# Kernel tuning notes

Measured on AMD Instinct MI355X. Metric: run time of the kernel, lower is better.

Reference implementation:

```python
import math
import jax, jax.numpy as jnp
import numpy as np

HIDDEN = 1024
HEADS = 16
HEAD = HIDDEN // HEADS
BUCKET = 32
MAXPOS = 512
REL = 2 * BUCKET - 1
EPS = 1e-7
L, B = 512, 16
STD = math.sqrt(2.0 / (5.0 * HIDDEN))


def _ln(x, g=None, b=None):
    m = x.mean(-1, keepdims=True)
    v = ((x - m) ** 2).mean(-1, keepdims=True)
    y = (x - m) * jax.lax.rsqrt(v + EPS)
    return y if g is None else y * g + b


def _bucket_indices(n):
    # DeBERTa-style log bucket relative positions, shifted to [0, 2*BUCKET-2]
    r = jnp.arange(n)[:, None] - jnp.arange(n)[None, :]
    mid = BUCKET // 2
    abs_pos = jnp.where((r < mid) & (r > -mid), mid - 1,
                        jnp.clip(jnp.abs(r), None, MAXPOS - 1))
    log_pos = jnp.ceil(jnp.log(abs_pos.astype(jnp.float32) / mid)
                       / math.log((MAXPOS - 1) / mid) * (mid - 1)).astype(jnp.int32) + mid
    bucket_pos = jnp.where(abs_pos <= mid, r, log_pos * jnp.sign(r))
    return (BUCKET - 1 + bucket_pos).astype(jnp.int32)


def setup_inputs() -> dict:
    key = jax.random.key(0)
    ks = jax.random.split(key, 8)
    return {
        'hidden_states': jax.random.normal(ks[0], (L, B, HIDDEN), jnp.float32),
        'attention_mask': jax.random.randint(ks[1], (B, 1, 1, L), 0, 2).astype(bool),
        'relative_embedding': jax.random.normal(ks[2], (REL, HIDDEN), jnp.float32),
        'wqk': jax.random.normal(ks[3], (2 * HIDDEN, HIDDEN), jnp.float32) * STD,
        'bqk': jnp.zeros((2 * HIDDEN,), jnp.float32),
        'wv': jax.random.normal(ks[4], (HIDDEN, HIDDEN), jnp.float32) * STD,
        'bv': jnp.zeros((HIDDEN,), jnp.float32),
        'wo': jax.random.normal(ks[5], (HIDDEN, HIDDEN), jnp.float32) * STD,
        'bo': jnp.zeros((HIDDEN,), jnp.float32),
        'ln_g': jnp.ones((HIDDEN,), jnp.float32),
        'ln_b': jnp.zeros((HIDDEN,), jnp.float32),
    }


def reference(hidden_states, attention_mask, relative_embedding,
              wqk, bqk, wv, bv, wo, bo, ln_g, ln_b):
    Lq, Bq, D = hidden_states.shape
    scale = 1.0 / math.sqrt(3 * HEAD)
    h = _ln(hidden_states)                                 # pre LN, no affine
    q, k = jnp.split(h @ wqk.T + bqk, 2, axis=-1)
    v = h @ wv.T + bv
    qpos, kpos = jnp.split(relative_embedding @ wqk.T + bqk, 2, axis=-1)
    qpos = qpos.reshape(REL, HEADS, HEAD)
    kpos = kpos.reshape(REL, HEADS, HEAD)
    # (L,B,D) -> (B,H,L,hd)
    qh = q.reshape(Lq, Bq, HEADS, HEAD).transpose(1, 2, 0, 3)
    kh = k.reshape(Lq, Bq, HEADS, HEAD).transpose(1, 2, 0, 3)
    vh = v.reshape(Lq, Bq, HEADS, HEAD).transpose(1, 2, 0, 3)
    scores = jnp.einsum('bhqd,bhkd->bhqk', qh, kh) * scale       # c2c
    qp = jnp.einsum('bhqd,khd->bhqk', qh, kpos) * scale          # c2p (k over buckets)
    pk = jnp.einsum('bhkd,qhd->bhqk', kh, qpos) * scale          # p2c (q over buckets)
    idx = jnp.broadcast_to(_bucket_indices(Lq), (Bq, HEADS, Lq, Lq))
    scores = scores + jnp.take_along_axis(qp, idx, axis=-1) \
                    + jnp.take_along_axis(pk, idx, axis=-2)
    # masked softmax: mask==True -> -inf before softmax, 0 after
    probs = jax.nn.softmax(jnp.where(attention_mask, -1e9, scores), axis=-1)
    probs = jnp.where(attention_mask, 0.0, probs)
    ctx = jnp.einsum('bhqk,bhkd->bhqd', probs, vh)
    ctx = ctx.transpose(2, 0, 1, 3).reshape(Lq, Bq, D)           # (L,B,D)
    out = ctx @ wo.T + bo
    return _ln(out, ln_g, ln_b)
```

## Files before the change

### kernel.cpp

```cpp
#include <hip/hip_runtime.h>
#include <hip/hip_bf16.h>

#define HID 1024
#define HEADS 16
#define HEAD 64
#define RELN 63
#define SEQ 512
#define BATCH 16
#define NROWS (SEQ*BATCH)
#define MEXT 8320
#define NQKV 3072
#define LNEPS 1e-7f

typedef __attribute__((ext_vector_type(4))) float  f32x4;
typedef __attribute__((ext_vector_type(8))) short  s16x8;
typedef __attribute__((ext_vector_type(4))) ushort u16x4;

static __device__ __forceinline__ ushort f2bf(float f) {
  union { float f; unsigned u; } v; v.f = f;
  unsigned r = v.u + 0x7fffu + ((v.u >> 16) & 1u);
  return (ushort)(r >> 16);
}
static __device__ __forceinline__ float bf2f(ushort u) {
  union { unsigned u; float f; } v; v.u = ((unsigned)u) << 16;
  return v.f;
}

__global__ void k_prep(const void* mask_raw, const float* bqk, const float* bv,
                       ushort* mask01, int* idx_tab, float* bcat) {
  __shared__ int s_isbool;
  int tid = threadIdx.x;
  if (tid == 0) s_isbool = 0;
  __syncthreads();
  const unsigned* mu = (const unsigned*)mask_raw;
  int bad = 0;
  for (int i = tid; i < 2048; i += 256) if (mu[i] > 1u) bad = 1;
  if (bad) s_isbool = 1;
  __syncthreads();
  int isbool = s_isbool;
  const unsigned char* m8 = (const unsigned char*)mask_raw;
  const int* m32 = (const int*)mask_raw;
  for (int i = tid; i < BATCH*SEQ; i += 256) {
    int m = isbool ? (int)m8[i] : m32[i];
    mask01[i] = m ? 1 : 0;
  }
  for (int i = tid; i < 1023; i += 256) {
    int r = i - 511;
    int a = r < 0 ? -r : r;
    int absp = (a < 16) ? 15 : (a < 511 ? a : 511);
    int idx;
    if (absp <= 16) idx = 31 + r;
    else {
      float v = logf((float)absp / 16.0f) / logf(511.0f / 16.0f) * 15.0f;
      int lp = (int)ceilf(v) + 16;
      idx = 31 + (r > 0 ? lp : -lp);
    }
    idx_tab[i] = idx;
  }
  for (int i = tid; i < 2048; i += 256) bcat[i] = bqk[i];
  for (int i = tid; i < 1024; i += 256) bcat[2048 + i] = bv[i];
}

__global__ void k_convert(const float* wqk, const float* wv, const float* wo,
                          ushort* wcat, ushort* wo_b) {
  int i = blockIdx.x * 256 + threadIdx.x;
  if (i < 2048 * 1024) wcat[i] = f2bf(wqk[i]);
  else if (i < 3072 * 1024) wcat[i] = f2bf(wv[i - 2048 * 1024]);
  if (i < 1024 * 1024) wo_b[i] = f2bf(wo[i]);
}

__global__ __launch_bounds__(256) void k_ln1(const float* hid, const float* rel, ushort* h_ext) {
  int row = blockIdx.x, tid = threadIdx.x;
  __shared__ float red[8];
  if (row < NROWS) {
    const float* src = hid + (size_t)row * HID;
    f32x4 x = *(const f32x4*)(src + tid * 4);
    float s = x[0] + x[1] + x[2] + x[3];
    #pragma unroll
    for (int m = 1; m < 64; m <<= 1) s += __shfl_xor(s, m);
    if ((tid & 63) == 0) red[tid >> 6] = s;
    __syncthreads();
    float mean = (red[0] + red[1] + red[2] + red[3]) * (1.0f / HID);
    float d0 = x[0] - mean, d1 = x[1] - mean, d2 = x[2] - mean, d3 = x[3] - mean;
    float sq = d0*d0 + d1*d1 + d2*d2 + d3*d3;
    #pragma unroll
    for (int m = 1; m < 64; m <<= 1) sq += __shfl_xor(sq, m);
    __syncthreads();
    if ((tid & 63) == 0) red[4 + (tid >> 6)] = sq;
    __syncthreads();
    float var = (red[4] + red[5] + red[6] + red[7]) * (1.0f / HID);
    float rs = rsqrtf(var + LNEPS);
    u16x4 o = { f2bf(d0*rs), f2bf(d1*rs), f2bf(d2*rs), f2bf(d3*rs) };
    *(u16x4*)(h_ext + (size_t)row * HID + tid * 4) = o;
  } else if (row < NROWS + RELN) {
    const float* src = rel + (size_t)(row - NROWS) * HID;
    f32x4 x = *(const f32x4*)(src + tid * 4);
    u16x4 o = { f2bf(x[0]), f2bf(x[1]), f2bf(x[2]), f2bf(x[3]) };
    *(u16x4*)(h_ext + (size_t)row * HID + tid * 4) = o;
  } else {
    u16x4 z = { 0, 0, 0, 0 };
    *(u16x4*)(h_ext + (size_t)row * HID + tid * 4) = z;
  }
}

template<int WRITE_F32>
__global__ __launch_bounds__(256) void k_gemm(const ushort* A, const ushort* Bw, const float* bias,
                                              ushort* Cb, float* Cf, int M, int N, int K) {
  __shared__ char smem[32768];
  char* As = smem;
  char* Bs = smem + 16384;
  int tid = threadIdx.x, lane = tid & 63, w = tid >> 6;
  int nbn = N >> 7;
  int per = gridDim.x >> 3;
  int gl = (blockIdx.x & 7) * per + (blockIdx.x >> 3);
  int bm = gl / nbn, bn = gl % nbn;
  int wr = w >> 1, wc = w & 1;
  int g = lane >> 4, r = lane & 15;
  f32x4 acc[4][4] = {};
  for (int ko = 0; ko < K; ko += 64) {
    __syncthreads();
    #pragma unroll
    for (int c = 0; c < 4; ++c) {
      int chunk = c * 256 + tid;
      int row = chunk >> 3;
      int kb = (chunk & 7) << 4;
      int kbs = kb ^ ((row & 7) << 4);
      const char* gA = (const char*)(A + (size_t)(bm * 128 + row) * K + ko) + kbs;
      const char* gB = (const char*)(Bw + (size_t)(bn * 128 + row) * K + ko) + kbs;
      __builtin_amdgcn_global_load_lds((const __attribute__((address_space(1))) void*)gA,
                                       (__attribute__((address_space(3))) void*)(As + c * 4096 + w * 1024),
                                       16, 0, 0);
      __builtin_amdgcn_global_load_lds((const __attribute__((address_space(1))) void*)gB,
                                       (__attribute__((address_space(3))) void*)(Bs + c * 4096 + w * 1024),
                                       16, 0, 0);
    }
    __syncthreads();
    #pragma unroll
    for (int kk = 0; kk < 2; ++kk) {
      s16x8 af[4], bf[4];
      #pragma unroll
      for (int mt = 0; mt < 4; ++mt) {
        int row = wr * 64 + mt * 16 + r;
        int kb = (kk * 64 + g * 16) ^ ((row & 7) << 4);
        af[mt] = *(const s16x8*)(As + row * 128 + kb);
      }
      #pragma unroll
      for (int nt = 0; nt < 4; ++nt) {
        int row = wc * 64 + nt * 16 + r;
        int kb = (kk * 64 + g * 16) ^ ((row & 7) << 4);
        bf[nt] = *(const s16x8*)(Bs + row * 128 + kb);
      }
      #pragma unroll
      for (int mt = 0; mt < 4; ++mt)
        #pragma unroll
        for (int nt = 0; nt < 4; ++nt)
          acc[mt][nt] = __builtin_amdgcn_mfma_f32_16x16x32_bf16(af[mt], bf[nt], acc[mt][nt], 0, 0, 0);
    }
  }
  #pragma unroll
  for (int nt = 0; nt < 4; ++nt) {
    int col = bn * 128 + wc * 64 + nt * 16 + r;
    float bvv = bias[col];
    #pragma unroll
    for (int mt = 0; mt < 4; ++mt) {
      int row0 = bm * 128 + wr * 64 + mt * 16 + g * 4;
      #pragma unroll
      for (int i = 0; i < 4; ++i) {
        float v = acc[mt][nt][i] + bvv;
        if (WRITE_F32) Cf[(size_t)(row0 + i) * N + col] = v;
        else           Cb[(size_t)(row0 + i) * N + col] = f2bf(v);
      }
    }
  }
}

__global__ __launch_bounds__(256) void k_pos(const ushort* qkv, ushort* qp, ushort* pk) {
  int bh = blockIdx.x;
  int b = bh >> 4, h = bh & 15;
  int tid = threadIdx.x, lane = tid & 63, w = tid >> 6;
  int g = lane >> 4, r = lane & 15;
  s16x8 bkp[4][2], bqp[4][2];
  #pragma unroll
  for (int nt = 0; nt < 4; ++nt)
    #pragma unroll
    for (int kk = 0; kk < 2; ++kk) {
      size_t rowp = (size_t)(NROWS + nt * 16 + r);
      int colq = h * 64 + kk * 32 + g * 8;
      bqp[nt][kk] = *(const s16x8*)(qkv + rowp * NQKV + colq);
      bkp[nt][kk] = *(const s16x8*)(qkv + rowp * NQKV + 1024 + colq);
    }
  for (int cc = 0; cc < 8; ++cc) {
    int rowbase = cc * 64 + w * 16;
    s16x8 aq[2], ak[2];
    #pragma unroll
    for (int kk = 0; kk < 2; ++kk) {
      size_t rowq = (size_t)((rowbase + r) * 16 + b);
      int colq = h * 64 + kk * 32 + g * 8;
      aq[kk] = *(const s16x8*)(qkv + rowq * NQKV + colq);
      ak[kk] = *(const s16x8*)(qkv + rowq * NQKV + 1024 + colq);
    }
    f32x4 accq[4] = {}, acck[4] = {};
    #pragma unroll
    for (int kk = 0; kk < 2; ++kk)
      #pragma unroll
      for (int nt = 0; nt < 4; ++nt) {
        accq[nt] = __builtin_amdgcn_mfma_f32_16x16x32_bf16(aq[kk], bkp[nt][kk], accq[nt], 0, 0, 0);
        acck[nt] = __builtin_amdgcn_mfma_f32_16x16x32_bf16(ak[kk], bqp[nt][kk], acck[nt], 0, 0, 0);
      }
    #pragma unroll
    for (int nt = 0; nt < 4; ++nt)
      #pragma unroll
      for (int i = 0; i < 4; ++i) {
        int q = rowbase + g * 4 + i;
        int t = nt * 16 + r;
        qp[(size_t)bh * SEQ * 64 + q * 64 + t] = f2bf(accq[nt][i]);
        pk[(size_t)bh * SEQ * 64 + q * 64 + t] = f2bf(acck[nt][i]);
      }
  }
}

__global__ __launch_bounds__(256) void k_vt(const ushort* qkv, ushort* vt, ushort* kc) {
  int bid = blockIdx.x;
  int bh = bid >> 3, lt = bid & 7;
  int b = bh >> 4, h = bh & 15;
  __shared__ ushort tile[64][72];
  int tid = threadIdx.x;
  #pragma unroll
  for (int c = 0; c < 2; ++c) {
    int e = (c * 256 + tid) * 8;
    int l = e >> 6, d0 = e & 63;
    size_t row = (size_t)((lt * 64 + l) * 16 + b);
    s16x8 kv = *(const s16x8*)(qkv + row * NQKV + 1024 + h * 64 + d0);
    *(s16x8*)(kc + ((size_t)bh * SEQ + lt * 64 + l) * 64 + d0) = kv;
    *(s16x8*)&tile[l][d0] = *(const s16x8*)(qkv + row * NQKV + 2048 + h * 64 + d0);
  }
  __syncthreads();
  #pragma unroll
  for (int c = 0; c < 2; ++c) {
    int e = (c * 256 + tid) * 8;
    int d = e >> 6, l0 = e & 63;
    ushort tmp[8];
    #pragma unroll
    for (int j = 0; j < 8; ++j) tmp[j] = tile[l0 + j][d];
    *(s16x8*)(vt + (size_t)(bh * 64 + d) * SEQ + lt * 64 + l0) = *(s16x8*)tmp;
  }
}

__global__ __launch_bounds__(256) void k_attn(const ushort* qkv, const ushort* qp_all, const ushort* pk_all,
                                              const ushort* kc, const ushort* vt, const ushort* mask01,
                                              const int* idx_tab, ushort* ctx) {
  int bid = blockIdx.x;
  int slot = bid >> 3;
  int bh = (bid & 7) * 32 + (slot >> 3);
  int qt = slot & 7;
  int b = bh >> 4, h = bh & 15;
  int tid = threadIdx.x, lane = tid & 63, w = tid >> 6;
  int g = lane >> 4, r = lane & 15;

  __shared__ ushort qp_s[64][66];
  __shared__ ushort pk_s[2][64][66];
  __shared__ char   Ks[2][8192];
  __shared__ ushort p_s[4][16][72];
  __shared__ ushort mb_s[512];
  __shared__ ushort idx_s[1024];
  char* Ksp = (char*)Ks;

  const size_t qp_base = (size_t)bh * SEQ * 64 + (size_t)qt * 4096;
  const size_t pk_base = (size_t)bh * SEQ * 64;
  const char* kcb = (const char*)(kc + (size_t)bh * SEQ * 64);

  int krow = w * 8 + (lane >> 3);
  int ksrccol = (((lane & 7) ^ (lane >> 3)) << 4);

  #pragma unroll
  for (int c = 0; c < 2; ++c) {
    const char* src = kcb + (size_t)(c * 32 + krow) * 128 + ksrccol;
    __builtin_amdgcn_global_load_lds((const __attribute__((address_space(1))) void*)src,
                                     (__attribute__((address_space(3))) void*)(Ksp + c * 4096 + w * 1024),
                                     16, 0, 0);
  }
  s16x8 pkreg[2];
  #pragma unroll
  for (int c = 0; c < 2; ++c)
    pkreg[c] = *(const s16x8*)(pk_all + pk_base + (size_t)(c * 256 + tid) * 8);
  #pragma unroll
  for (int c = 0; c < 2; ++c) {
    int chunk = c * 256 + tid;
    s16x8 v = *(const s16x8*)(qp_all + qp_base + (size_t)chunk * 8);
    *(s16x8*)&qp_s[chunk >> 3][(chunk & 7) * 8] = v;
  }
  for (int i = tid; i < 512; i += 256) mb_s[i] = mask01[b * SEQ + i];
  for (int i = tid; i < 1023; i += 256) idx_s[i] = (ushort)idx_tab[i];
  s16x8 aq[2];
  int qg0 = qt * 64 + w * 16;
  #pragma unroll
  for (int kk = 0; kk < 2; ++kk) {
    size_t row = (size_t)((qg0 + r) * 16 + b);
    aq[kk] = *(const s16x8*)(qkv + row * NQKV + h * 64 + kk * 32 + g * 8);
  }
  #pragma unroll
  for (int c = 0; c < 2; ++c) {
    int chunk = c * 256 + tid;
    *(s16x8*)&pk_s[0][chunk >> 3][(chunk & 7) * 8] = pkreg[c];
  }
  __syncthreads();

  float m_i[4], l_i[4];
  f32x4 o_acc[4] = {};
  #pragma unroll
  for (int i = 0; i < 4; ++i) { m_i[i] = -3e38f; l_i[i] = 0.0f; }
  const float scale = 0.07216878364870323f;

  #pragma unroll 2
  for (int kt = 0; kt < 8; ++kt) {
    const int cur = kt & 1;
    if (kt < 7) {
      #pragma unroll
      for (int c = 0; c < 2; ++c) {
        const char* src = kcb + (size_t)(kt + 1) * 8192 + (size_t)(c * 32 + krow) * 128 + ksrccol;
        __builtin_amdgcn_global_load_lds((const __attribute__((address_space(1))) void*)src,
                                         (__attribute__((address_space(3))) void*)(Ksp + (cur ^ 1) * 8192 + c * 4096 + w * 1024),
                                         16, 0, 0);
      }
      #pragma unroll
      for (int c = 0; c < 2; ++c)
        pkreg[c] = *(const s16x8*)(pk_all + pk_base + (size_t)(kt + 1) * 4096 + (size_t)(c * 256 + tid) * 8);
    }

    const char* Kc = Ksp + cur * 8192;
    f32x4 s[4];
    #pragma unroll
    for (int nt = 0; nt < 4; ++nt) {
      f32x4 a = {};
      #pragma unroll
      for (int kk = 0; kk < 2; ++kk) {
        s16x8 bk = *(const s16x8*)(Kc + (nt * 16 + r) * 128 + ((kk * 64 + g * 16) ^ ((r & 7) << 4)));
        a = __builtin_amdgcn_mfma_f32_16x16x32_bf16(aq[kk], bk, a, 0, 0, 0);
      }
      s[nt] = a;
    }

    s16x8 vreg[2][4];
    #pragma unroll
    for (int kk = 0; kk < 2; ++kk)
      #pragma unroll
      for (int nt = 0; nt < 4; ++nt)
        vreg[kk][nt] = *(const s16x8*)(vt + (size_t)(bh * 64 + nt * 16 + r) * SEQ + kt * 64 + kk * 32 + g * 8);

    float p[4][4], tilemax[4];
    #pragma unroll
    for (int i = 0; i < 4; ++i) tilemax[i] = -3e38f;
    #pragma unroll
    for (int nt = 0; nt < 4; ++nt) {
      int kl = nt * 16 + r;
      int kgl = kt * 64 + kl;
      ushort mb = mb_s[kgl];
      #pragma unroll
      for (int i = 0; i < 4; ++i) {
        int ql = w * 16 + g * 4 + i;
        int ridx = (qt * 64 + ql) - kgl + 511;
        int t = idx_s[ridx];
        float v = (s[nt][i] + bf2f(qp_s[ql][t]) + bf2f(pk_s[cur][kl][t])) * scale;
        v = mb ? -3e38f : v;
        s[nt][i] = v;
        tilemax[i] = fmaxf(tilemax[i], v);
      }
    }
    #pragma unroll
    for (int i = 0; i < 4; ++i) {
      float v = tilemax[i];
      v = fmaxf(v, __shfl_xor(v, 1));
      v = fmaxf(v, __shfl_xor(v, 2));
      v = fmaxf(v, __shfl_xor(v, 4));
      v = fmaxf(v, __shfl_xor(v, 8));
      tilemax[i] = v;
    }
    float rs_i[4], psum[4];
    #pragma unroll
    for (int i = 0; i < 4; ++i) {
      float mnew = fmaxf(m_i[i], tilemax[i]);
      rs_i[i] = __expf(m_i[i] - mnew);
      m_i[i] = mnew;
      l_i[i] *= rs_i[i];
      psum[i] = 0.0f;
    }
    #pragma unroll
    for (int nt = 0; nt < 4; ++nt)
      #pragma unroll
      for (int i = 0; i < 4; ++i) {
        float v = s[nt][i];
        float pe = (v <= -1e37f) ? 0.0f : __expf(v - m_i[i]);
        p[nt][i] = pe;
        psum[i] += pe;
      }
    #pragma unroll
    for (int i = 0; i < 4; ++i) {
      float v = psum[i];
      v += __shfl_xor(v, 1);
      v += __shfl_xor(v, 2);
      v += __shfl_xor(v, 4);
      v += __shfl_xor(v, 8);
      l_i[i] += v;
    }
    #pragma unroll
    for (int nt = 0; nt < 4; ++nt)
      #pragma unroll
      for (int i = 0; i < 4; ++i) o_acc[nt][i] *= rs_i[i];

    #pragma unroll
    for (int nt = 0; nt < 4; ++nt)
      #pragma unroll
      for (int i = 0; i < 4; ++i) p_s[w][g * 4 + i][nt * 16 + r] = f2bf(p[nt][i]);

    #pragma unroll
    for (int kk = 0; kk < 2; ++kk) {
      s16x8 pa = *(const s16x8*)&p_s[w][r][kk * 32 + g * 8];
      #pragma unroll
      for (int nt = 0; nt < 4; ++nt)
        o_acc[nt] = __builtin_amdgcn_mfma_f32_16x16x32_bf16(pa, vreg[kk][nt], o_acc[nt], 0, 0, 0);
    }

    if (kt < 7) {
      #pragma unroll
      for (int c = 0; c < 2; ++c) {
        int chunk = c * 256 + tid;
        *(s16x8*)&pk_s[cur ^ 1][chunk >> 3][(chunk & 7) * 8] = pkreg[c];
      }
    }
    __syncthreads();
  }

  #pragma unroll
  for (int i = 0; i < 4; ++i) {
    float inv = l_i[i] > 0.0f ? 1.0f / l_i[i] : 0.0f;
    int lq = qt * 64 + w * 16 + g * 4 + i;
    size_t rowc = (size_t)(lq * 16 + b);
    #pragma unroll
    for (int nt = 0; nt < 4; ++nt)
      ctx[rowc * HID + h * 64 + nt * 16 + r] = f2bf(o_acc[nt][i] * inv);
  }
}

__global__ __launch_bounds__(256) void k_ln2(const float* tmp, const float* gamma, const float* beta,
                                             float* out) {
  int row = blockIdx.x, tid = threadIdx.x;
  __shared__ float red[8];
  const float* src = tmp + (size_t)row * HID;
  f32x4 x = *(const f32x4*)(src + tid * 4);
  float s = x[0] + x[1] + x[2] + x[3];
  #pragma unroll
  for (int m = 1; m < 64; m <<= 1) s += __shfl_xor(s, m);
  if ((tid & 63) == 0) red[tid >> 6] = s;
  __syncthreads();
  float mean = (red[0] + red[1] + red[2] + red[3]) * (1.0f / HID);
  float d[4]; float sq = 0.0f;
  #pragma unroll
  for (int j = 0; j < 4; ++j) { d[j] = x[j] - mean; sq += d[j] * d[j]; }
  #pragma unroll
  for (int m = 1; m < 64; m <<= 1) sq += __shfl_xor(sq, m);
  __syncthreads();
  if ((tid & 63) == 0) red[4 + (tid >> 6)] = sq;
  __syncthreads();
  float var = (red[4] + red[5] + red[6] + red[7]) * (1.0f / HID);
  float rs = rsqrtf(var + LNEPS);
  f32x4 o;
  #pragma unroll
  for (int j = 0; j < 4; ++j) o[j] = d[j] * rs * gamma[tid * 4 + j] + beta[tid * 4 + j];
  *(f32x4*)(out + (size_t)row * HID + tid * 4) = o;
}

extern "C" void kernel_launch(void* const* d_in, const int* in_sizes, int n_in,
                              void* d_out, int out_size, void* d_ws, size_t ws_size,
                              hipStream_t stream) {
  (void)in_sizes; (void)n_in; (void)out_size; (void)ws_size;
  const float* hid  = (const float*)d_in[0];
  const void*  mask = d_in[1];
  const float* rel  = (const float*)d_in[2];
  const float* wqk  = (const float*)d_in[3];
  const float* bqk  = (const float*)d_in[4];
  const float* wv   = (const float*)d_in[5];
  const float* bv   = (const float*)d_in[6];
  const float* wo   = (const float*)d_in[7];
  const float* bo   = (const float*)d_in[8];
  const float* ln_g = (const float*)d_in[9];
  const float* ln_b = (const float*)d_in[10];

  char* ws = (char*)d_ws;
  ushort* wcat     = (ushort*)(ws);
  ushort* wo_b     = (ushort*)(ws + 6291456);
  float*  bcat     = (float*) (ws + 8388608);
  ushort* mask01   = (ushort*)(ws + 8400896);
  int*    idx_tab  = (int*)   (ws + 8433664);
  ushort* h_ext    = (ushort*)(ws + 8437760);
  ushort* qkv      = (ushort*)(ws + 25477120);
  ushort* qp_b     = (ushort*)(ws + 76595200);
  ushort* pk_b     = (ushort*)(ws + 93372416);
  ushort* vt       = (ushort*)(ws + 110149632);
  float*  tmp      = (float*) (ws + 126926848);
  ushort* ctx = h_ext;
  ushort* kc  = (ushort*)tmp;

  k_prep<<<1, 256, 0, stream>>>(mask, bqk, bv, mask01, idx_tab, bcat);
  k_convert<<<12288, 256, 0, stream>>>(wqk, wv, wo, wcat, wo_b);
  k_ln1<<<MEXT, 256, 0, stream>>>(hid, rel, h_ext);
  k_gemm<0><<<(MEXT / 128) * (NQKV / 128), 256, 0, stream>>>(h_ext, wcat, bcat, qkv, nullptr, MEXT, NQKV, 1024);
  k_pos<<<256, 256, 0, stream>>>(qkv, qp_b, pk_b);
  k_vt<<<2048, 256, 0, stream>>>(qkv, vt, kc);
  k_attn<<<2048, 256, 0, stream>>>(qkv, qp_b, pk_b, kc, vt, mask01, idx_tab, ctx);
  k_gemm<1><<<(NROWS / 128) * (1024 / 128), 256, 0, stream>>>(ctx, wo_b, bo, nullptr, tmp, NROWS, 1024, 1024);
  k_ln2<<<NROWS, 256, 0, stream>>>(tmp, ln_g, ln_b, (float*)d_out);
}
```

Before: 290.8 us.

## Fold softmax scale and key mask into precomputed operands; single-buffer K tile

The attention scale is applied ahead of time: K is pre-scaled in k_vt, and the qp/pk tables are scaled in k_pos. The key mask becomes a -1e9 additive bias baked into the pk table, which removes the per-element scale multiply, the mask lookup and the masked-exp branch from the attention inner loop. The K and pk tiles in LDS drop from double to single buffering with an extra mid-loop barrier, and idx_s shrinks to bytes, cutting LDS use in exchange for less load/compute overlap. Pre-scaling K in bf16 adds one more rounding step.

```diff
diff --git a/kernel.cpp b/kernel.cpp
--- a/kernel.cpp
+++ b/kernel.cpp
@@ -11,6 +11,7 @@
 #define MEXT 8320
 #define NQKV 3072
 #define LNEPS 1e-7f
+#define SCALEF 0.07216878364870323f
 
 typedef __attribute__((ext_vector_type(4))) float  f32x4;
 typedef __attribute__((ext_vector_type(8))) short  s16x8;
@@ -174,11 +175,15 @@
   }
 }
 
-__global__ __launch_bounds__(256) void k_pos(const ushort* qkv, ushort* qp, ushort* pk) {
+__global__ __launch_bounds__(256) void k_pos(const ushort* qkv, const ushort* mask01,
+                                             ushort* qp, ushort* pk) {
   int bh = blockIdx.x;
   int b = bh >> 4, h = bh & 15;
   int tid = threadIdx.x, lane = tid & 63, w = tid >> 6;
   int g = lane >> 4, r = lane & 15;
+  __shared__ ushort mb[512];
+  for (int i = tid; i < 512; i += 256) mb[i] = mask01[b * SEQ + i];
+  __syncthreads();
   s16x8 bkp[4][2], bqp[4][2];
   #pragma unroll
   for (int nt = 0; nt < 4; ++nt)
@@ -213,8 +218,9 @@
       for (int i = 0; i < 4; ++i) {
         int q = rowbase + g * 4 + i;
         int t = nt * 16 + r;
-        qp[(size_t)bh * SEQ * 64 + q * 64 + t] = f2bf(accq[nt][i]);
-        pk[(size_t)bh * SEQ * 64 + q * 64 + t] = f2bf(acck[nt][i]);
+        float biasv = mb[q] ? -1e9f : 0.0f;
+        qp[(size_t)bh * SEQ * 64 + q * 64 + t] = f2bf(accq[nt][i] * SCALEF);
+        pk[(size_t)bh * SEQ * 64 + q * 64 + t] = f2bf(acck[nt][i] * SCALEF + biasv);
       }
   }
 }
@@ -231,6 +237,8 @@
     int l = e >> 6, d0 = e & 63;
     size_t row = (size_t)((lt * 64 + l) * 16 + b);
     s16x8 kv = *(const s16x8*)(qkv + row * NQKV + 1024 + h * 64 + d0);
+    #pragma unroll
+    for (int j = 0; j < 8; ++j) kv[j] = (short)f2bf(bf2f((ushort)kv[j]) * SCALEF);
     *(s16x8*)(kc + ((size_t)bh * SEQ + lt * 64 + l) * 64 + d0) = kv;
     *(s16x8*)&tile[l][d0] = *(const s16x8*)(qkv + row * NQKV + 2048 + h * 64 + d0);
   }
@@ -247,7 +255,7 @@
 }
 
 __global__ __launch_bounds__(256) void k_attn(const ushort* qkv, const ushort* qp_all, const ushort* pk_all,
-                                              const ushort* kc, const ushort* vt, const ushort* mask01,
+                                              const ushort* kc, const ushort* vt,
                                               const int* idx_tab, ushort* ctx) {
   int bid = blockIdx.x;
   int slot = bid >> 3;
@@ -257,26 +265,24 @@
   int tid = threadIdx.x, lane = tid & 63, w = tid >> 6;
   int g = lane >> 4, r = lane & 15;
 
-  __shared__ ushort qp_s[64][66];
-  __shared__ ushort pk_s[2][64][66];
-  __shared__ char   Ks[2][8192];
+  __shared__ char   Ks[8192];
+  __shared__ ushort qp_s[64][72];
+  __shared__ ushort pk_s[64][72];
   __shared__ ushort p_s[4][16][72];
-  __shared__ ushort mb_s[512];
-  __shared__ ushort idx_s[1024];
-  char* Ksp = (char*)Ks;
+  __shared__ unsigned char idx_s[1024];
 
   const size_t qp_base = (size_t)bh * SEQ * 64 + (size_t)qt * 4096;
   const size_t pk_base = (size_t)bh * SEQ * 64;
   const char* kcb = (const char*)(kc + (size_t)bh * SEQ * 64);
 
   int krow = w * 8 + (lane >> 3);
-  int ksrccol = (((lane & 7) ^ (lane >> 3)) << 4);
+  int ksrccol = ((lane & 7) ^ (lane >> 3)) << 4;
 
   #pragma unroll
   for (int c = 0; c < 2; ++c) {
     const char* src = kcb + (size_t)(c * 32 + krow) * 128 + ksrccol;
     __builtin_amdgcn_global_load_lds((const __attribute__((address_space(1))) void*)src,
-                                     (__attribute__((address_space(3))) void*)(Ksp + c * 4096 + w * 1024),
+                                     (__attribute__((address_space(3))) void*)(Ks + c * 4096 + w * 1024),
                                      16, 0, 0);
   }
   s16x8 pkreg[2];
@@ -289,8 +295,7 @@
     s16x8 v = *(const s16x8*)(qp_all + qp_base + (size_t)chunk * 8);
     *(s16x8*)&qp_s[chunk >> 3][(chunk & 7) * 8] = v;
   }
-  for (int i = tid; i < 512; i += 256) mb_s[i] = mask01[b * SEQ + i];
-  for (int i = tid; i < 1023; i += 256) idx_s[i] = (ushort)idx_tab[i];
+  for (int i = tid; i < 1023; i += 256) idx_s[i] = (unsigned char)idx_tab[i];
   s16x8 aq[2];
   int qg0 = qt * 64 + w * 16;
   #pragma unroll
@@ -301,7 +306,7 @@
   #pragma unroll
   for (int c = 0; c < 2; ++c) {
     int chunk = c * 256 + tid;
-    *(s16x8*)&pk_s[0][chunk >> 3][(chunk & 7) * 8] = pkreg[c];
+    *(s16x8*)&pk_s[chunk >> 3][(chunk & 7) * 8] = pkreg[c];
   }
   __syncthreads();
 
@@ -309,37 +314,58 @@
   f32x4 o_acc[4] = {};
   #pragma unroll
   for (int i = 0; i < 4; ++i) { m_i[i] = -3e38f; l_i[i] = 0.0f; }
-  const float scale = 0.07216878364870323f;
-
-  #pragma unroll 2
+
   for (int kt = 0; kt < 8; ++kt) {
-    const int cur = kt & 1;
+    if (kt < 7) {
+      #pragma unroll
+      for (int c = 0; c < 2; ++c)
+        pkreg[c] = *(const s16x8*)(pk_all + pk_base + (size_t)(kt + 1) * 4096 + (size_t)(c * 256 + tid) * 8);
+    }
+
+    f32x4 s[4];
+    #pragma unroll
+    for (int nt = 0; nt < 4; ++nt) {
+      f32x4 a = {};
+      #pragma unroll
+      for (int kk = 0; kk < 2; ++kk) {
+        s16x8 bk = *(const s16x8*)(Ks + (nt * 16 + r) * 128 + ((kk * 64 + g * 16) ^ ((r & 7) << 4)));
+        a = __builtin_amdgcn_mfma_f32_16x16x32_bf16(aq[kk], bk, a, 0, 0, 0);
+      }
+      s[nt] = a;
+    }
+
+    float tilemax[4];
+    #pragma unroll
+    for (int i = 0; i < 4; ++i) tilemax[i] = -3e38f;
+    #pragma unroll
+    for (int nt = 0; nt < 4; ++nt) {
+      int kl = nt * 16 + r;
+      int kgl = kt * 64 + kl;
+      #pragma unroll
+      for (int i = 0; i < 4; ++i) {
+        int ql = w * 16 + g * 4 + i;
+        int t = idx_s[(qt * 64 + ql) - kgl + 511];
+        float v = s[nt][i] + bf2f(qp_s[ql][t]) + bf2f(pk_s[kl][t]);
+        s[nt][i] = v;
+        tilemax[i] = fmaxf(tilemax[i], v);
+      }
+    }
+    __syncthreads();
+
     if (kt < 7) {
       #pragma unroll
       for (int c = 0; c < 2; ++c) {
         const char* src = kcb + (size_t)(kt + 1) * 8192 + (size_t)(c * 32 + krow) * 128 + ksrccol;
         __builtin_amdgcn_global_load_lds((const __attribute__((address_space(1))) void*)src,
-                                         (__attribute__((address_space(3))) void*)(Ksp + (cur ^ 1) * 8192 + c * 4096 + w * 1024),
+                                         (__attribute__((address_space(3))) void*)(Ks + c * 4096 + w * 1024),
                                          16, 0, 0);
       }
       #pragma unroll
-      for (int c = 0; c < 2; ++c)
-        pkreg[c] = *(const s16x8*)(pk_all + pk_base + (size_t)(kt + 1) * 4096 + (size_t)(c * 256 + tid) * 8);
-    }
-
-    const char* Kc = Ksp + cur * 8192;
-    f32x4 s[4];
-    #pragma unroll
-    for (int nt = 0; nt < 4; ++nt) {
-      f32x4 a = {};
-      #pragma unroll
-      for (int kk = 0; kk < 2; ++kk) {
-        s16x8 bk = *(const s16x8*)(Kc + (nt * 16 + r) * 128 + ((kk * 64 + g * 16) ^ ((r & 7) << 4)));
-        a = __builtin_amdgcn_mfma_f32_16x16x32_bf16(aq[kk], bk, a, 0, 0, 0);
-      }
-      s[nt] = a;
-    }
-
+      for (int c = 0; c < 2; ++c) {
+        int chunk = c * 256 + tid;
+        *(s16x8*)&pk_s[chunk >> 3][(chunk & 7) * 8] = pkreg[c];
+      }
+    }
     s16x8 vreg[2][4];
     #pragma unroll
     for (int kk = 0; kk < 2; ++kk)
@@ -347,25 +373,6 @@
       for (int nt = 0; nt < 4; ++nt)
         vreg[kk][nt] = *(const s16x8*)(vt + (size_t)(bh * 64 + nt * 16 + r) * SEQ + kt * 64 + kk * 32 + g * 8);
 
-    float p[4][4], tilemax[4];
-    #pragma unroll
-    for (int i = 0; i < 4; ++i) tilemax[i] = -3e38f;
-    #pragma unroll
-    for (int nt = 0; nt < 4; ++nt) {
-      int kl = nt * 16 + r;
-      int kgl = kt * 64 + kl;
-      ushort mb = mb_s[kgl];
-      #pragma unroll
-      for (int i = 0; i < 4; ++i) {
-        int ql = w * 16 + g * 4 + i;
-        int ridx = (qt * 64 + ql) - kgl + 511;
-        int t = idx_s[ridx];
-        float v = (s[nt][i] + bf2f(qp_s[ql][t]) + bf2f(pk_s[cur][kl][t])) * scale;
-        v = mb ? -3e38f : v;
-        s[nt][i] = v;
-        tilemax[i] = fmaxf(tilemax[i], v);
-      }
-    }
     #pragma unroll
     for (int i = 0; i < 4; ++i) {
       float v = tilemax[i];
@@ -388,10 +395,9 @@
     for (int nt = 0; nt < 4; ++nt)
       #pragma unroll
       for (int i = 0; i < 4; ++i) {
-        float v = s[nt][i];
-        float pe = (v <= -1e37f) ? 0.0f : __expf(v - m_i[i]);
-        p[nt][i] = pe;
+        float pe = __expf(s[nt][i] - m_i[i]);
         psum[i] += pe;
+        p_s[w][g * 4 + i][nt * 16 + r] = f2bf(pe);
       }
     #pragma unroll
     for (int i = 0; i < 4; ++i) {
@@ -408,11 +414,6 @@
       for (int i = 0; i < 4; ++i) o_acc[nt][i] *= rs_i[i];
 
     #pragma unroll
-    for (int nt = 0; nt < 4; ++nt)
-      #pragma unroll
-      for (int i = 0; i < 4; ++i) p_s[w][g * 4 + i][nt * 16 + r] = f2bf(p[nt][i]);
-
-    #pragma unroll
     for (int kk = 0; kk < 2; ++kk) {
       s16x8 pa = *(const s16x8*)&p_s[w][r][kk * 32 + g * 8];
       #pragma unroll
@@ -420,14 +421,7 @@
         o_acc[nt] = __builtin_amdgcn_mfma_f32_16x16x32_bf16(pa, vreg[kk][nt], o_acc[nt], 0, 0, 0);
     }
 
-    if (kt < 7) {
-      #pragma unroll
-      for (int c = 0; c < 2; ++c) {
-        int chunk = c * 256 + tid;
-        *(s16x8*)&pk_s[cur ^ 1][chunk >> 3][(chunk & 7) * 8] = pkreg[c];
-      }
-    }
-    __syncthreads();
+    if (kt < 7) __syncthreads();
   }
 
   #pragma unroll
@@ -504,9 +498,9 @@
   k_convert<<<12288, 256, 0, stream>>>(wqk, wv, wo, wcat, wo_b);
   k_ln1<<<MEXT, 256, 0, stream>>>(hid, rel, h_ext);
   k_gemm<0><<<(MEXT / 128) * (NQKV / 128), 256, 0, stream>>>(h_ext, wcat, bcat, qkv, nullptr, MEXT, NQKV, 1024);
-  k_pos<<<256, 256, 0, stream>>>(qkv, qp_b, pk_b);
+  k_pos<<<256, 256, 0, stream>>>(qkv, mask01, qp_b, pk_b);
   k_vt<<<2048, 256, 0, stream>>>(qkv, vt, kc);
-  k_attn<<<2048, 256, 0, stream>>>(qkv, qp_b, pk_b, kc, vt, mask01, idx_tab, ctx);
+  k_attn<<<2048, 256, 0, stream>>>(qkv, qp_b, pk_b, kc, vt, idx_tab, ctx);
   k_gemm<1><<<(NROWS / 128) * (1024 / 128), 256, 0, stream>>>(ctx, wo_b, bo, nullptr, tmp, NROWS, 1024, 1024);
   k_ln2<<<NROWS, 256, 0, stream>>>(tmp, ln_g, ln_b, (float*)d_out);
 }
```

New measurement: 266.9 us. -8.2%, faster.
